# Performance work log

Hardware: AMD Instinct MI355X
Metric: run time of the kernel (lower is better)

The kernel has to match this reference:

```python
import jax, jax.numpy as jnp
import numpy as np

B = 8192
NUM_NODES = 100000
EMB = 128
W1D, W2D, W3D = 64, 128, 256   # witness_dims
CODE = 128
HID = 64                        # hardcoded hidden_dim in WitnessExtractor / decoder
TOTW = W1D + W2D + W3D          # 448


def _linear_params(key, fan_in, fan_out):
    k1, k2 = jax.random.split(key)
    bound = 1.0 / np.sqrt(fan_in)
    w = jax.random.uniform(k1, (fan_out, fan_in), jnp.float32, -bound, bound)
    b = jax.random.uniform(k2, (fan_out,), jnp.float32, -bound, bound)
    return w, b


def setup_inputs() -> dict:
    key = jax.random.key(0)
    ks = jax.random.split(key, 12)
    u = jax.random.randint(ks[0], (B,), 0, NUM_NODES, dtype=jnp.int64 if jax.config.jax_enable_x64 else jnp.int32)
    v = jax.random.randint(ks[1], (B,), 0, NUM_NODES, dtype=u.dtype)
    emb = jax.random.normal(ks[2], (NUM_NODES, EMB), jnp.float32)
    e1_w1, e1_b1 = _linear_params(ks[3], 2 * EMB, HID)
    e1_w2, e1_b2 = _linear_params(ks[4], HID, W1D)
    e2_w1, e2_b1 = _linear_params(ks[5], 2 * EMB + W1D, HID)
    e2_w2, e2_b2 = _linear_params(ks[6], HID, W2D)
    e3_w1, e3_b1 = _linear_params(ks[7], 2 * EMB + W2D, HID)
    e3_w2, e3_b2 = _linear_params(ks[8], HID, W3D)
    trop_w = jax.random.normal(ks[9], (CODE, TOTW), jnp.float32)  # init_scale=1.0
    dec_w1, dec_b1 = _linear_params(ks[10], CODE, HID)
    dec_w2, dec_b2 = _linear_params(ks[11], HID, 1)
    return dict(u=u, v=v, emb=emb,
                e1_w1=e1_w1, e1_b1=e1_b1, e1_w2=e1_w2, e1_b2=e1_b2,
                e2_w1=e2_w1, e2_b1=e2_b1, e2_w2=e2_w2, e2_b2=e2_b2,
                e3_w1=e3_w1, e3_b1=e3_b1, e3_w2=e3_w2, e3_b2=e3_b2,
                trop_w=trop_w, dec_w1=dec_w1, dec_b1=dec_b1,
                dec_w2=dec_w2, dec_b2=dec_b2)


def _witness(x, w1, b1, w2, b2):
    h = jax.nn.relu(x @ w1.T + b1)
    return jax.nn.sigmoid(h @ w2.T + b2)


def reference(u, v, emb,
              e1_w1, e1_b1, e1_w2, e1_b2,
              e2_w1, e2_b1, e2_w2, e2_b2,
              e3_w1, e3_b1, e3_w2, e3_b2,
              trop_w, dec_w1, dec_b1, dec_w2, dec_b2):
    u_emb = emb[u]                               # [B, EMB]
    v_emb = emb[v]
    base = jnp.concatenate([u_emb, v_emb], axis=1)  # [B, 2*EMB]
    w1 = _witness(base, e1_w1, e1_b1, e1_w2, e1_b2)
    w2 = _witness(jnp.concatenate([base, w1], axis=1), e2_w1, e2_b1, e2_w2, e2_b2)
    w3 = _witness(jnp.concatenate([base, w2], axis=1), e3_w1, e3_b1, e3_w2, e3_b2)
    wit = jnp.concatenate([w1, w2, w3], axis=1)  # [B, TOTW]
    # tropical (min-plus) matmul: code[b,o] = min_j (wit[b,j] + trop_w[o,j])
    code = jnp.min(wit[:, None, :] + trop_w[None, :, :], axis=2)  # [B, CODE]
    h = jax.nn.relu(code @ dec_w1.T + dec_b1)
    return h @ dec_w2.T + dec_b2                 # [B, 1]
```

## Files before the change

### kernel.cpp

```cpp
#include <hip/hip_runtime.h>
#include <hip/hip_fp16.h>
#include <math.h>

#define BATCH 8192
#define EMB 128
#define TILE 16
#define NTHREADS 1024
#define NWAVES 16
#define CH 136
#define WITS 450
#define ENT_CAP 4096

#define OFF_E1W1 0
#define OFF_E1W2 16384
#define OFF_E2W1 20480
#define OFF_E2W2 40960
#define OFF_E3W1 49152
#define OFF_E3W2 73728
#define OFF_DW1  90112
#define OFF_DW2  98304
#define W_DENSE  98368

typedef __attribute__((ext_vector_type(8))) _Float16 v8h;
typedef __attribute__((ext_vector_type(4))) float v4f;

struct Smem {
    _Float16 XB[32 * CH];
    _Float16 W12C[24 * CH];
    _Float16 H[8 * CH];
    _Float16 CODE[16 * CH];
    _Float16 WITrm[TILE * WITS];
    unsigned int ent[ENT_CAP];
    unsigned int off[132];
};

__global__ __launch_bounds__(1024) void prep_kernel(
    const float* __restrict__ s0, const float* __restrict__ s1,
    const float* __restrict__ s2, const float* __restrict__ s3,
    const float* __restrict__ s4, const float* __restrict__ s5,
    const float* __restrict__ s6, const float* __restrict__ s7,
    const float* __restrict__ trop, _Float16* __restrict__ ws)
{
    const int b = blockIdx.x;
    const int tid = threadIdx.x;
    if (b < 25) {
        const int idx4 = (b * 1024 + tid) * 4;
        if (idx4 >= W_DENSE) return;
        const float* src; int off;
        if      (idx4 < OFF_E1W2) { src = s0; off = OFF_E1W1; }
        else if (idx4 < OFF_E2W1) { src = s1; off = OFF_E1W2; }
        else if (idx4 < OFF_E2W2) { src = s2; off = OFF_E2W1; }
        else if (idx4 < OFF_E3W1) { src = s3; off = OFF_E2W2; }
        else if (idx4 < OFF_E3W2) { src = s4; off = OFF_E3W1; }
        else if (idx4 < OFF_DW1)  { src = s5; off = OFF_E3W2; }
        else if (idx4 < OFF_DW2)  { src = s6; off = OFF_DW1;  }
        else                      { src = s7; off = OFF_DW2;  }
        const float4 v = *(const float4*)(src + (idx4 - off));
        _Float16* dst = ws + idx4;
        dst[0] = (_Float16)v.x; dst[1] = (_Float16)v.y;
        dst[2] = (_Float16)v.z; dst[3] = (_Float16)v.w;
    } else {
        const int lane = tid & 63;
        const int wave = tid >> 6;
        const int o = (b - 25) * 16 + wave;
        if (o >= 128) return;
        unsigned int* base = (unsigned int*)(ws + W_DENSE);
        unsigned int* counter = base + 131;

        const float* row = trop + (size_t)o * 448;
        float vals[7];
        float mn = 1e30f;
        #pragma unroll
        for (int it = 0; it < 7; ++it) {
            vals[it] = row[lane + it * 64];
            mn = fminf(mn, vals[it]);
        }
        mn = fminf(mn, __shfl_xor(mn, 1, 64));
        mn = fminf(mn, __shfl_xor(mn, 2, 64));
        mn = fminf(mn, __shfl_xor(mn, 4, 64));
        mn = fminf(mn, __shfl_xor(mn, 8, 64));
        mn = fminf(mn, __shfl_xor(mn, 16, 64));
        mn = fminf(mn, __shfl_xor(mn, 32, 64));
        const float thr = mn + 1.02f;

        unsigned long long masks[7];
        unsigned int n = 0;
        #pragma unroll
        for (int it = 0; it < 7; ++it) {
            masks[it] = __ballot(vals[it] <= thr);
            n += (unsigned)__popcll(masks[it]);
        }
        unsigned int beg = 0;
        if (lane == 0) beg = atomicAdd(counter, n);
        beg = (unsigned)__shfl((int)beg, 0, 64);
        if (lane == 0) base[o] = (n << 16) | (beg & 0xffffu);

        unsigned int done = beg;
        const unsigned long long ltmask = (1ull << lane) - 1ull;
        #pragma unroll
        for (int it = 0; it < 7; ++it) {
            const unsigned long long m = masks[it];
            if (vals[it] <= thr) {
                const unsigned int pos = done + (unsigned)__popcll(m & ltmask);
                if (pos < ENT_CAP) {
                    const unsigned short hb =
                        __builtin_bit_cast(unsigned short, (_Float16)vals[it]);
                    base[132 + pos] = ((unsigned)(lane + it * 64) << 16) | hb;
                }
            }
            done += (unsigned)__popcll(m);
        }
    }
}

template <int K, int STEPS0, int O, int ACT, bool CHUNKW, bool RMW>
__device__ __forceinline__ void dense_mfma(
    const _Float16* __restrict__ Wg, const float* __restrict__ bias,
    const _Float16* A0, const _Float16* A1,
    _Float16* OutC, _Float16* OutRM, int rmbase, int wave, int lane)
{
    constexpr int STEPS = K / 32;
    static_assert(STEPS % 2 == 0, "even steps");
    constexpr int NJOBS = O / 16;
    const int l15 = lane & 15;
    const int quad = lane >> 4;

    for (int nt = wave; nt < NJOBS; nt += NWAVES) {
        v4f c0 = {0.f, 0.f, 0.f, 0.f};
        v4f c1 = {0.f, 0.f, 0.f, 0.f};
        const _Float16* wrow = Wg + (size_t)(nt * 16 + l15) * K + quad * 8;
        #pragma unroll
        for (int s = 0; s < STEPS; s += 2) {
            const int g0 = s * 4 + quad;
            const int g1 = (s + 1) * 4 + quad;
            const _Float16* a0p = (s < STEPS0)
                ? (A0 + g0 * CH + l15 * 8)
                : (A1 + (g0 - STEPS0 * 4) * CH + l15 * 8);
            const _Float16* a1p = ((s + 1) < STEPS0)
                ? (A0 + g1 * CH + l15 * 8)
                : (A1 + (g1 - STEPS0 * 4) * CH + l15 * 8);
            const v8h a0 = *(const v8h*)a0p;
            const v8h b0 = *(const v8h*)(wrow + s * 32);
            const v8h a1 = *(const v8h*)a1p;
            const v8h b1 = *(const v8h*)(wrow + (s + 1) * 32);
            c0 = __builtin_amdgcn_mfma_f32_16x16x32_f16(a0, b0, c0, 0, 0, 0);
            c1 = __builtin_amdgcn_mfma_f32_16x16x32_f16(a1, b1, c1, 0, 0, 0);
        }
        const v4f c = c0 + c1;
        const int o = nt * 16 + l15;
        const float bs = bias[o];
        #pragma unroll
        for (int i = 0; i < 4; ++i) {
            float vv = c[i] + bs;
            if (ACT == 0) vv = fmaxf(vv, 0.f);
            else          vv = 1.f / (1.f + __expf(-vv));
            const int m = quad * 4 + i;
            const _Float16 hv = (_Float16)vv;
            if (CHUNKW) OutC[(o >> 3) * CH + m * 8 + (o & 7)] = hv;
            if (RMW)    OutRM[m * WITS + rmbase + o] = hv;
        }
    }
}

__global__ __launch_bounds__(NTHREADS, 8) void tacit_fused_kernel(
    const int* __restrict__ u, const int* __restrict__ v,
    const float* __restrict__ emb,
    const float* __restrict__ e1_b1, const float* __restrict__ e1_b2,
    const float* __restrict__ e2_b1, const float* __restrict__ e2_b2,
    const float* __restrict__ e3_b1, const float* __restrict__ e3_b2,
    const float* __restrict__ dec_b1, const float* __restrict__ dec_b2,
    const _Float16* __restrict__ ws,
    float* __restrict__ out)
{
    __shared__ Smem S;
    const int tid = threadIdx.x;
    const int lane = tid & 63;
    const int wave = tid >> 6;
    const int row0 = blockIdx.x * TILE;

    {
        const unsigned int* base = (const unsigned int*)(ws + W_DENSE);
        if (tid < 33) *(uint4*)&S.off[tid * 4] = *(const uint4*)(base + tid * 4);
        *(uint4*)&S.ent[tid * 4] = *(const uint4*)(base + 132 + tid * 4);
    }
    if (tid < 512) {
        const int row = tid & 15;
        const int kq = tid >> 4;
        const int node = (kq < 16) ? u[row0 + row] : v[row0 + row];
        const int col = (kq & 15) * 8;
        const float4 f0 = *(const float4*)(emb + (size_t)node * EMB + col);
        const float4 f1 = *(const float4*)(emb + (size_t)node * EMB + col + 4);
        v8h hv;
        hv[0] = (_Float16)f0.x; hv[1] = (_Float16)f0.y;
        hv[2] = (_Float16)f0.z; hv[3] = (_Float16)f0.w;
        hv[4] = (_Float16)f1.x; hv[5] = (_Float16)f1.y;
        hv[6] = (_Float16)f1.z; hv[7] = (_Float16)f1.w;
        *(v8h*)&S.XB[kq * CH + row * 8] = hv;
    }
    __syncthreads();

    dense_mfma<256, 8, 64, 0, true, false>(ws + OFF_E1W1, e1_b1, S.XB, nullptr,
                                           S.H, nullptr, 0, wave, lane);
    __syncthreads();
    dense_mfma<64, 2, 64, 1, true, true>(ws + OFF_E1W2, e1_b2, S.H, nullptr,
                                         S.W12C, S.WITrm, 0, wave, lane);
    __syncthreads();

    dense_mfma<320, 8, 64, 0, true, false>(ws + OFF_E2W1, e2_b1, S.XB, S.W12C,
                                           S.H, nullptr, 0, wave, lane);
    __syncthreads();
    dense_mfma<64, 2, 128, 1, true, true>(ws + OFF_E2W2, e2_b2, S.H, nullptr,
                                          S.W12C + 8 * CH, S.WITrm, 64, wave, lane);
    __syncthreads();

    dense_mfma<384, 8, 64, 0, true, false>(ws + OFF_E3W1, e3_b1, S.XB, S.W12C + 8 * CH,
                                           S.H, nullptr, 0, wave, lane);
    __syncthreads();
    dense_mfma<64, 2, 256, 1, false, true>(ws + OFF_E3W2, e3_b2, S.H, nullptr,
                                           nullptr, S.WITrm, 192, wave, lane);
    __syncthreads();

    {
        const int r = lane & 15;
        const int cp = lane >> 4;
        const _Float16* wrow = &S.WITrm[r * WITS];
        float acc[8];
        int idx[8], end8[8];
        #pragma unroll
        for (int i = 0; i < 8; ++i) {
            const int o = (wave << 3) + i;
            const unsigned int tb = S.off[o];
            const int beg = (int)(tb & 0xffffu);
            int e = beg + (int)(tb >> 16);
            e = e < ENT_CAP ? e : ENT_CAP;
            idx[i] = beg + cp;
            end8[i] = e;
            acc[i] = 1e30f;
        }
        bool any = true;
        while (any) {
            any = false;
            #pragma unroll
            for (int i = 0; i < 8; ++i) {
                if (idx[i] < end8[i]) {
                    const unsigned int cwv = S.ent[idx[i]];
                    const int j = (int)(cwv >> 16);
                    const float tv = (float)__builtin_bit_cast(
                        _Float16, (unsigned short)(cwv & 0xffffu));
                    acc[i] = fminf(acc[i], (float)wrow[j] + tv);
                    idx[i] += 4;
                    any = true;
                }
            }
        }
        #pragma unroll
        for (int i = 0; i < 8; ++i) {
            float a = acc[i];
            a = fminf(a, __shfl_xor(a, 16, 64));
            a = fminf(a, __shfl_xor(a, 32, 64));
            if (cp == 0) {
                const int o = (wave << 3) + i;
                S.CODE[(o >> 3) * CH + r * 8 + (o & 7)] = (_Float16)a;
            }
        }
    }
    __syncthreads();

    dense_mfma<128, 4, 64, 0, true, false>(ws + OFF_DW1, dec_b1, S.CODE, nullptr,
                                           S.H, nullptr, 0, wave, lane);
    __syncthreads();

    if (tid < 64) {
        const int r = lane & 15;
        const int part = lane >> 4;
        const _Float16* w2 = ws + OFF_DW2;
        float s = 0.f;
        #pragma unroll
        for (int q = 0; q < 2; ++q) {
            const int c = part + q * 4;
            const v8h hr = *(const v8h*)(&S.H[c * CH + r * 8]);
            const v8h wr = *(const v8h*)(w2 + c * 8);
            #pragma unroll
            for (int t = 0; t < 8; ++t) s += (float)hr[t] * (float)wr[t];
        }
        s += __shfl_xor(s, 16, 64);
        s += __shfl_xor(s, 32, 64);
        if (part == 0) out[row0 + r] = s + dec_b2[0];
    }
}

extern "C" void kernel_launch(void* const* d_in, const int* in_sizes, int n_in,
                              void* d_out, int out_size, void* d_ws, size_t ws_size,
                              hipStream_t stream) {
    const int*   u      = (const int*)d_in[0];
    const int*   v      = (const int*)d_in[1];
    const float* emb    = (const float*)d_in[2];
    const float* e1_w1  = (const float*)d_in[3];
    const float* e1_b1  = (const float*)d_in[4];
    const float* e1_w2  = (const float*)d_in[5];
    const float* e1_b2  = (const float*)d_in[6];
    const float* e2_w1  = (const float*)d_in[7];
    const float* e2_b1  = (const float*)d_in[8];
    const float* e2_w2  = (const float*)d_in[9];
    const float* e2_b2  = (const float*)d_in[10];
    const float* e3_w1  = (const float*)d_in[11];
    const float* e3_b1  = (const float*)d_in[12];
    const float* e3_w2  = (const float*)d_in[13];
    const float* e3_b2  = (const float*)d_in[14];
    const float* trop_w = (const float*)d_in[15];
    const float* dec_w1 = (const float*)d_in[16];
    const float* dec_b1 = (const float*)d_in[17];
    const float* dec_w2 = (const float*)d_in[18];
    const float* dec_b2 = (const float*)d_in[19];
    float* out = (float*)d_out;
    _Float16* ws = (_Float16*)d_ws;

    hipMemsetAsync((char*)d_ws + (size_t)W_DENSE * 2 + 131 * 4, 0, 4, stream);

    prep_kernel<<<33, 1024, 0, stream>>>(
        e1_w1, e1_w2, e2_w1, e2_w2, e3_w1, e3_w2, dec_w1, dec_w2, trop_w, ws);

    tacit_fused_kernel<<<BATCH / TILE, NTHREADS, 0, stream>>>(
        u, v, emb,
        e1_b1, e1_b2, e2_b1, e2_b2, e3_b1, e3_b2, dec_b1, dec_b2,
        ws, out);
}
```

Baseline: 144.7 us.

## Build tropical candidate lists per block in shared memory, drop memset and atomics

The fused kernel now builds the pruned candidate list for each tropical output itself. Each wave scans 8 rows of trop_w and writes up to 32 entries per output into fixed shared-memory slots. If an output has more than 32 candidates, it falls back to a full 448-element scan. This removes the workspace memset, the prep-kernel blocks that did the selection, and the global atomic offset, so one launch/memset goes away. The cost is that every block re-reads all of trop_w from L2 and spends time on selection before the first matmul, although some of that may overlap with the embedding gather.

```diff
diff --git a/kernel.cpp b/kernel.cpp
--- a/kernel.cpp
+++ b/kernel.cpp
@@ -9,7 +9,7 @@
 #define NWAVES 16
 #define CH 136
 #define WITS 450
-#define ENT_CAP 4096
+#define SLOT 32
 
 #define OFF_E1W1 0
 #define OFF_E1W2 16384
@@ -30,8 +30,8 @@
     _Float16 H[8 * CH];
     _Float16 CODE[16 * CH];
     _Float16 WITrm[TILE * WITS];
-    unsigned int ent[ENT_CAP];
-    unsigned int off[132];
+    unsigned int ent[128 * SLOT];
+    unsigned int cnt[128];
 };
 
 __global__ __launch_bounds__(1024) void prep_kernel(
@@ -39,78 +39,23 @@
     const float* __restrict__ s2, const float* __restrict__ s3,
     const float* __restrict__ s4, const float* __restrict__ s5,
     const float* __restrict__ s6, const float* __restrict__ s7,
-    const float* __restrict__ trop, _Float16* __restrict__ ws)
+    _Float16* __restrict__ ws)
 {
-    const int b = blockIdx.x;
-    const int tid = threadIdx.x;
-    if (b < 25) {
-        const int idx4 = (b * 1024 + tid) * 4;
-        if (idx4 >= W_DENSE) return;
-        const float* src; int off;
-        if      (idx4 < OFF_E1W2) { src = s0; off = OFF_E1W1; }
-        else if (idx4 < OFF_E2W1) { src = s1; off = OFF_E1W2; }
-        else if (idx4 < OFF_E2W2) { src = s2; off = OFF_E2W1; }
-        else if (idx4 < OFF_E3W1) { src = s3; off = OFF_E2W2; }
-        else if (idx4 < OFF_E3W2) { src = s4; off = OFF_E3W1; }
-        else if (idx4 < OFF_DW1)  { src = s5; off = OFF_E3W2; }
-        else if (idx4 < OFF_DW2)  { src = s6; off = OFF_DW1;  }
-        else                      { src = s7; off = OFF_DW2;  }
-        const float4 v = *(const float4*)(src + (idx4 - off));
-        _Float16* dst = ws + idx4;
-        dst[0] = (_Float16)v.x; dst[1] = (_Float16)v.y;
-        dst[2] = (_Float16)v.z; dst[3] = (_Float16)v.w;
-    } else {
-        const int lane = tid & 63;
-        const int wave = tid >> 6;
-        const int o = (b - 25) * 16 + wave;
-        if (o >= 128) return;
-        unsigned int* base = (unsigned int*)(ws + W_DENSE);
-        unsigned int* counter = base + 131;
-
-        const float* row = trop + (size_t)o * 448;
-        float vals[7];
-        float mn = 1e30f;
-        #pragma unroll
-        for (int it = 0; it < 7; ++it) {
-            vals[it] = row[lane + it * 64];
-            mn = fminf(mn, vals[it]);
-        }
-        mn = fminf(mn, __shfl_xor(mn, 1, 64));
-        mn = fminf(mn, __shfl_xor(mn, 2, 64));
-        mn = fminf(mn, __shfl_xor(mn, 4, 64));
-        mn = fminf(mn, __shfl_xor(mn, 8, 64));
-        mn = fminf(mn, __shfl_xor(mn, 16, 64));
-        mn = fminf(mn, __shfl_xor(mn, 32, 64));
-        const float thr = mn + 1.02f;
-
-        unsigned long long masks[7];
-        unsigned int n = 0;
-        #pragma unroll
-        for (int it = 0; it < 7; ++it) {
-            masks[it] = __ballot(vals[it] <= thr);
-            n += (unsigned)__popcll(masks[it]);
-        }
-        unsigned int beg = 0;
-        if (lane == 0) beg = atomicAdd(counter, n);
-        beg = (unsigned)__shfl((int)beg, 0, 64);
-        if (lane == 0) base[o] = (n << 16) | (beg & 0xffffu);
-
-        unsigned int done = beg;
-        const unsigned long long ltmask = (1ull << lane) - 1ull;
-        #pragma unroll
-        for (int it = 0; it < 7; ++it) {
-            const unsigned long long m = masks[it];
-            if (vals[it] <= thr) {
-                const unsigned int pos = done + (unsigned)__popcll(m & ltmask);
-                if (pos < ENT_CAP) {
-                    const unsigned short hb =
-                        __builtin_bit_cast(unsigned short, (_Float16)vals[it]);
-                    base[132 + pos] = ((unsigned)(lane + it * 64) << 16) | hb;
-                }
-            }
-            done += (unsigned)__popcll(m);
-        }
-    }
+    const int idx4 = (blockIdx.x * 1024 + threadIdx.x) * 4;
+    if (idx4 >= W_DENSE) return;
+    const float* src; int off;
+    if      (idx4 < OFF_E1W2) { src = s0; off = OFF_E1W1; }
+    else if (idx4 < OFF_E2W1) { src = s1; off = OFF_E1W2; }
+    else if (idx4 < OFF_E2W2) { src = s2; off = OFF_E2W1; }
+    else if (idx4 < OFF_E3W1) { src = s3; off = OFF_E2W2; }
+    else if (idx4 < OFF_E3W2) { src = s4; off = OFF_E3W1; }
+    else if (idx4 < OFF_DW1)  { src = s5; off = OFF_E3W2; }
+    else if (idx4 < OFF_DW2)  { src = s6; off = OFF_DW1;  }
+    else                      { src = s7; off = OFF_DW2;  }
+    const float4 v = *(const float4*)(src + (idx4 - off));
+    _Float16* dst = ws + idx4;
+    dst[0] = (_Float16)v.x; dst[1] = (_Float16)v.y;
+    dst[2] = (_Float16)v.z; dst[3] = (_Float16)v.w;
 }
 
 template <int K, int STEPS0, int O, int ACT, bool CHUNKW, bool RMW>
@@ -169,6 +114,7 @@
     const float* __restrict__ e2_b1, const float* __restrict__ e2_b2,
     const float* __restrict__ e3_b1, const float* __restrict__ e3_b2,
     const float* __restrict__ dec_b1, const float* __restrict__ dec_b2,
+    const float* __restrict__ trop,
     const _Float16* __restrict__ ws,
     float* __restrict__ out)
 {
@@ -178,11 +124,6 @@
     const int wave = tid >> 6;
     const int row0 = blockIdx.x * TILE;
 
-    {
-        const unsigned int* base = (const unsigned int*)(ws + W_DENSE);
-        if (tid < 33) *(uint4*)&S.off[tid * 4] = *(const uint4*)(base + tid * 4);
-        *(uint4*)&S.ent[tid * 4] = *(const uint4*)(base + 132 + tid * 4);
-    }
     if (tid < 512) {
         const int row = tid & 15;
         const int kq = tid >> 4;
@@ -197,6 +138,47 @@
         hv[6] = (_Float16)f1.z; hv[7] = (_Float16)f1.w;
         *(v8h*)&S.XB[kq * CH + row * 8] = hv;
     }
+
+    {
+        const unsigned long long ltmask = (1ull << lane) - 1ull;
+        #pragma unroll 1
+        for (int t = 0; t < 8; ++t) {
+            const int o = wave * 8 + t;
+            const float* row = trop + (size_t)o * 448;
+            float vals[7];
+            float mn = 1e30f;
+            #pragma unroll
+            for (int it = 0; it < 7; ++it) {
+                vals[it] = row[lane + it * 64];
+                mn = fminf(mn, vals[it]);
+            }
+            mn = fminf(mn, __shfl_xor(mn, 1, 64));
+            mn = fminf(mn, __shfl_xor(mn, 2, 64));
+            mn = fminf(mn, __shfl_xor(mn, 4, 64));
+            mn = fminf(mn, __shfl_xor(mn, 8, 64));
+            mn = fminf(mn, __shfl_xor(mn, 16, 64));
+            mn = fminf(mn, __shfl_xor(mn, 32, 64));
+            const float thr = mn + 1.02f;
+
+            unsigned int pos0 = 0;
+            #pragma unroll
+            for (int it = 0; it < 7; ++it) {
+                const bool sel = vals[it] <= thr;
+                const unsigned long long m = __ballot(sel);
+                if (sel) {
+                    const unsigned int pos = pos0 + (unsigned)__popcll(m & ltmask);
+                    if (pos < SLOT) {
+                        const unsigned short hb =
+                            __builtin_bit_cast(unsigned short, (_Float16)vals[it]);
+                        S.ent[o * SLOT + pos] =
+                            ((unsigned)(lane + it * 64) << 16) | hb;
+                    }
+                }
+                pos0 += (unsigned)__popcll(m);
+            }
+            if (lane == 0) S.cnt[o] = pos0;
+        }
+    }
     __syncthreads();
 
     dense_mfma<256, 8, 64, 0, true, false>(ws + OFF_E1W1, e1_b1, S.XB, nullptr,
@@ -229,12 +211,9 @@
         #pragma unroll
         for (int i = 0; i < 8; ++i) {
             const int o = (wave << 3) + i;
-            const unsigned int tb = S.off[o];
-            const int beg = (int)(tb & 0xffffu);
-            int e = beg + (int)(tb >> 16);
-            e = e < ENT_CAP ? e : ENT_CAP;
-            idx[i] = beg + cp;
-            end8[i] = e;
+            const int n = (int)S.cnt[o];
+            idx[i] = o * SLOT + cp;
+            end8[i] = o * SLOT + (n < SLOT ? n : SLOT);
             acc[i] = 1e30f;
         }
         bool any = true;
@@ -251,6 +230,15 @@
                     idx[i] += 4;
                     any = true;
                 }
+            }
+        }
+        #pragma unroll
+        for (int i = 0; i < 8; ++i) {
+            const int o = (wave << 3) + i;
+            if ((int)S.cnt[o] > SLOT) {
+                const float* trow = trop + (size_t)o * 448;
+                for (int j = cp; j < 448; j += 4)
+                    acc[i] = fminf(acc[i], (float)wrow[j] + trow[j]);
             }
         }
         #pragma unroll
@@ -315,13 +303,11 @@
     float* out = (float*)d_out;
     _Float16* ws = (_Float16*)d_ws;
 
-    hipMemsetAsync((char*)d_ws + (size_t)W_DENSE * 2 + 131 * 4, 0, 4, stream);
-
-    prep_kernel<<<33, 1024, 0, stream>>>(
-        e1_w1, e1_w2, e2_w1, e2_w2, e3_w1, e3_w2, dec_w1, dec_w2, trop_w, ws);
+    prep_kernel<<<25, 1024, 0, stream>>>(
+        e1_w1, e1_w2, e2_w1, e2_w2, e3_w1, e3_w2, dec_w1, dec_w2, ws);
 
     tacit_fused_kernel<<<BATCH / TILE, NTHREADS, 0, stream>>>(
         u, v, emb,
         e1_b1, e1_b2, e2_b1, e2_b2, e3_b1, e3_b2, dec_b1, dec_b2,
-        ws, out);
+        trop_w, ws, out);
 }
```

Result: slower. 157.9 us (+9.1%).
